# Kernel tuning notes

Hardware: AMD Instinct MI355X
Metric: run time of the kernel (lower is better)

Reference implementation:

```python
import jax, jax.numpy as jnp
import numpy as np

T = 2048
D_IN = 1024
D_OUT = 1024
N_HEAD = 16
HEAD_DIM = D_OUT // N_HEAD


def setup_inputs() -> dict:
    key = jax.random.key(0)
    kx, kq, kk, kv = jax.random.split(key, 4)
    s = 1.0 / np.sqrt(D_IN)
    return {
        "x": jax.random.normal(kx, (T, D_IN), dtype=jnp.float32),
        "W_q": jax.random.normal(kq, (D_OUT, D_IN), dtype=jnp.float32) * s,
        "W_k": jax.random.normal(kk, (D_OUT, D_IN), dtype=jnp.float32) * s,
        "W_v": jax.random.normal(kv, (D_OUT, D_IN), dtype=jnp.float32) * s,
    }


def reference(x, W_q, W_k, W_v):
    t = x.shape[0]
    # linear projections (torch Linear: y = x @ W.T), split into heads: [H, T, Dh]
    q = (x @ W_q.T).reshape(t, N_HEAD, HEAD_DIM).transpose(1, 0, 2)
    k = (x @ W_k.T).reshape(t, N_HEAD, HEAD_DIM).transpose(1, 0, 2)
    v = (x @ W_v.T).reshape(t, N_HEAD, HEAD_DIM).transpose(1, 0, 2)
    # raw scores [H, T, T]
    omega = jnp.einsum("hqd,hkd->hqk", q, k)
    causal = jnp.triu(jnp.ones((t, t), dtype=bool), k=1)
    omega = jnp.where(causal[None, :, :], -jnp.inf, omega)
    # NOTE: faithful to source quirk — divides by head_dim**(-0.5),
    # i.e. multiplies scores by sqrt(head_dim)
    att_w = jax.nn.softmax(omega * (HEAD_DIM ** 0.5), axis=-1)
    context = jnp.einsum("hqk,hkd->hqd", att_w, v)  # [H, T, Dh]
    return context.transpose(1, 0, 2).reshape(t, D_OUT)
```

## Files before the change

kernel.cpp:

```cpp
#include <hip/hip_runtime.h>
#include <hip/hip_bf16.h>


typedef __bf16 bf16x8 __attribute__((ext_vector_type(8)));
typedef __bf16 bf16x4 __attribute__((ext_vector_type(4)));
typedef float  f32x4  __attribute__((ext_vector_type(4)));
typedef float  f32x16 __attribute__((ext_vector_type(16)));
typedef unsigned int u32;
typedef u32 u32x2 __attribute__((ext_vector_type(2)));
typedef u32 u32x4 __attribute__((ext_vector_type(4)));

#define MFMA(a, b, c) __builtin_amdgcn_mfma_f32_16x16x32_bf16((a), (b), (c), 0, 0, 0)
#define MFMA32(a, b, c) __builtin_amdgcn_mfma_f32_32x32x16_bf16((a), (b), (c), 0, 0, 0)

#if __has_builtin(__builtin_amdgcn_exp2f)
#define EXP2F(x) __builtin_amdgcn_exp2f(x)
#else
#define EXP2F(x) exp2f(x)
#endif

constexpr int T = 2048, DIN = 1024, DOUT = 1024, NH = 16, DH = 64;
constexpr float SC = 11.5415603f;
constexpr float DEFER = 0.6931472f;

constexpr size_t SZ_XMAT = (size_t)T * DIN * 2;
constexpr size_t SZ_WMAT = (size_t)DOUT * DIN * 2;
constexpr size_t OFF_XH = 0;
constexpr size_t OFF_XL = OFF_XH + SZ_XMAT;
constexpr size_t OFF_QH = OFF_XL + SZ_XMAT;
constexpr size_t OFF_QL = OFF_QH + SZ_XMAT;
constexpr size_t OFF_KH = OFF_QL + SZ_XMAT;
constexpr size_t OFF_KL = OFF_KH + SZ_XMAT;
constexpr size_t OFF_VT = OFF_KL + SZ_XMAT;
constexpr size_t OFF_W  = OFF_VT + SZ_XMAT;

__device__ __forceinline__ void gload_lds16(const void* g, void* l) {
  __builtin_amdgcn_global_load_lds(
      (const __attribute__((address_space(1))) void*)g,
      (__attribute__((address_space(3))) void*)l, 16, 0, 0);
}

__device__ __forceinline__ float xor32f(float x, int hi) {
#if __has_builtin(__builtin_amdgcn_permlane32_swap)
  const u32 xu = __builtin_bit_cast(u32, x);
  const u32x2 rp = __builtin_amdgcn_permlane32_swap(xu, xu, false, false);
  return __builtin_bit_cast(float, hi ? rp[0] : rp[1]);
#else
  return __shfl_xor(x, 32, 64);
#endif
}

__global__ void split_all(const float* __restrict__ x, const float* __restrict__ wq,
                          const float* __restrict__ wk, const float* __restrict__ wv,
                          char* __restrict__ ws) {
  const int i = blockIdx.x * 256 + threadIdx.x;
  const float* src;
  __bf16 *hi, *lo;
  int off;
  if (i < T * DIN / 4) {
    src = x; off = i;
    hi = (__bf16*)(ws + OFF_XH);
    lo = (__bf16*)(ws + OFF_XL);
  } else {
    const int j = i - T * DIN / 4;
    const int z = j >> 18;
    off = j & 262143;
    src = (z == 0) ? wq : ((z == 1) ? wk : wv);
    hi = (__bf16*)(ws + OFF_W + (size_t)z * 2 * SZ_WMAT);
    lo = hi + (size_t)DOUT * DIN;
  }
  const f32x4 v = ((const f32x4*)src)[off];
  bf16x4 h, l;
#pragma unroll
  for (int j = 0; j < 4; ++j) {
    const float xv = v[j];
    const __bf16 hh = (__bf16)xv;
    h[j] = hh;
    l[j] = (__bf16)(xv - (float)hh);
  }
  ((bf16x4*)hi)[off] = h;
  ((bf16x4*)lo)[off] = l;
}

template <bool SPLIT>
__device__ __forceinline__ void proj_loop(const __bf16* __restrict__ Ah,
                                          const __bf16* __restrict__ Al,
                                          const __bf16* __restrict__ Bh,
                                          const __bf16* __restrict__ Bl,
                                          __bf16* lds, int tm, int tn, int lane,
                                          int wv, f32x4 (&acc)[4][4]) {
  constexpr int BUF = SPLIT ? 16384 : 8192;
  constexpr int BOFF = SPLIT ? 8192 : 4096;
  const int wm = wv >> 1, wn = wv & 1;
  const int q4 = lane >> 4, r16 = lane & 15;

  auto STAGE = [&](int ks, int buf) {
    const int k0 = ks * 32;
    __bf16* base = lds + buf * BUF;
#pragma unroll
    for (int j = 0; j < 2; ++j) {
      const int cbase = wv * 128 + j * 64;
      const int cidx = cbase + lane;
      const int row = cidx & 127, kc = cidx >> 7;
      const size_t ga = (size_t)(tm + row) * DIN + k0 + kc * 8;
      const size_t gb = (size_t)(tn + row) * DIN + k0 + kc * 8;
      gload_lds16(Ah + ga, base + cbase * 8);
      gload_lds16(Bh + gb, base + BOFF + cbase * 8);
      if constexpr (SPLIT) {
        gload_lds16(Al + ga, base + 4096 + cbase * 8);
        gload_lds16(Bl + gb, base + 12288 + cbase * 8);
      }
    }
  };

  STAGE(0, 0);
  STAGE(1, 1);

  for (int ks = 0; ks < 32; ++ks) {
    const int buf = ks & 1;
    if (ks < 31) {
      if constexpr (SPLIT) asm volatile("s_waitcnt vmcnt(8)" ::: "memory");
      else                 asm volatile("s_waitcnt vmcnt(4)" ::: "memory");
    } else {
      asm volatile("s_waitcnt vmcnt(0)" ::: "memory");
    }
    __builtin_amdgcn_s_barrier();
    __builtin_amdgcn_sched_barrier(0);

    const __bf16* ldsA = lds + buf * BUF;
    const __bf16* ldsB = ldsA + BOFF;

    bf16x8 fah[4], fbh[4], fal[4], fbl[4];
#pragma unroll
    for (int b = 0; b < 4; ++b) {
      const int ra = wm * 64 + b * 16 + r16;
      const int rb = wn * 64 + b * 16 + r16;
      fah[b] = *(const bf16x8*)(ldsA + (q4 * 128 + ra) * 8);
      fbh[b] = *(const bf16x8*)(ldsB + (q4 * 128 + rb) * 8);
      if constexpr (SPLIT) {
        fal[b] = *(const bf16x8*)(ldsA + 4096 + (q4 * 128 + ra) * 8);
        fbl[b] = *(const bf16x8*)(ldsB + 4096 + (q4 * 128 + rb) * 8);
      }
    }
    __builtin_amdgcn_s_setprio(1);
#pragma unroll
    for (int bm = 0; bm < 4; ++bm)
#pragma unroll
      for (int bn = 0; bn < 4; ++bn) {
        acc[bm][bn] = MFMA(fah[bm], fbh[bn], acc[bm][bn]);
        if constexpr (SPLIT) {
          acc[bm][bn] = MFMA(fah[bm], fbl[bn], acc[bm][bn]);
          acc[bm][bn] = MFMA(fal[bm], fbh[bn], acc[bm][bn]);
        }
      }
    __builtin_amdgcn_s_setprio(0);
    asm volatile("s_waitcnt lgkmcnt(0)" ::: "memory");
    __builtin_amdgcn_sched_barrier(0);
    __builtin_amdgcn_s_barrier();
    __builtin_amdgcn_sched_barrier(0);
    if (ks < 30) STAGE(ks + 2, buf);
  }
}

__global__ __launch_bounds__(256, 2) void qkv_proj(char* ws) {
  const int nb = (blockIdx.x & 7) * 48 + (blockIdx.x >> 3);
  const int z = nb >> 7;
  const int t_ = nb & 127;
  const int tm = (t_ >> 3) * 128;
  const int tn = (t_ & 7) * 128;
  const int tid = threadIdx.x;
  const int lane = tid & 63, wv = tid >> 6;
  const int wm = wv >> 1, wn = wv & 1;
  const int q4 = lane >> 4, r16 = lane & 15;

  const __bf16* Ah = (const __bf16*)(ws + OFF_XH);
  const __bf16* Al = (const __bf16*)(ws + OFF_XL);
  const __bf16* Bh = (const __bf16*)(ws + OFF_W + (size_t)z * 2 * SZ_WMAT);
  const __bf16* Bl = Bh + (size_t)DOUT * DIN;

  __shared__ alignas(16) __bf16 lds[32768];

  f32x4 acc[4][4] = {};

  if (z < 2) {
    proj_loop<true>(Ah, Al, Bh, Bl, lds, tm, tn, lane, wv, acc);
    __bf16* Oh = (__bf16*)(ws + (z == 0 ? OFF_QH : OFF_KH));
    __bf16* Ol = (__bf16*)(ws + (z == 0 ? OFF_QL : OFF_KL));
#pragma unroll
    for (int bm = 0; bm < 4; ++bm)
#pragma unroll
      for (int bn = 0; bn < 4; ++bn)
#pragma unroll
        for (int r = 0; r < 4; ++r) {
          const int t = tm + wm * 64 + bm * 16 + q4 * 4 + r;
          const int n = tn + wn * 64 + bn * 16 + r16;
          const float v = acc[bm][bn][r];
          const __bf16 hh = (__bf16)v;
          Oh[(size_t)t * DOUT + n] = hh;
          Ol[(size_t)t * DOUT + n] = (__bf16)(v - (float)hh);
        }
  } else {
    proj_loop<false>(Ah, Al, Bh, Bl, lds, tm, tn, lane, wv, acc);
    __syncthreads();
    __bf16* tb = lds;
#pragma unroll
    for (int bm = 0; bm < 4; ++bm)
#pragma unroll
      for (int bn = 0; bn < 4; ++bn)
#pragma unroll
        for (int r = 0; r < 4; ++r) {
          const int tl = wm * 64 + bm * 16 + q4 * 4 + r;
          const int nl = wn * 64 + bn * 16 + r16;
          tb[(size_t)nl * 136 + tl] = (__bf16)acc[bm][bn][r];
        }
    __syncthreads();
    __bf16* Vt = (__bf16*)(ws + OFF_VT);
#pragma unroll
    for (int it = 0; it < 8; ++it) {
      const int cid = it * 256 + tid;
      const int nl = cid >> 4, tc = cid & 15;
      const bf16x8 vd = *(const bf16x8*)(tb + (size_t)nl * 136 + tc * 8);
      *(bf16x8*)(Vt + (size_t)(tn + nl) * T + tm + tc * 8) = vd;
    }
  }
}

__global__ __launch_bounds__(256, 2) void attn_kernel(const char* __restrict__ ws,
                                                      float* __restrict__ out) {
  const int bid = blockIdx.x;
  const int h = bid & 15;
  const int qt = (bid < 256) ? (31 - (bid >> 4)) : ((bid - 256) >> 4);
  const int tid = threadIdx.x;
  const int lane = tid & 63, wid = tid >> 6;
  const int qhalf = wid & 1, kvpar = wid >> 1;
  const int r32 = lane & 31, hi = lane >> 5, hi8 = hi * 8;
  const int qg = qt * 64 + qhalf * 32 + r32;
  const int NT = qt + 1;
  const int mid = (NT + 1) >> 1;
  const int tBeg = kvpar ? mid : 0;
  const int tEnd = kvpar ? NT : mid;

  const __bf16* Qh = (const __bf16*)(ws + OFF_QH);
  const __bf16* Ql = (const __bf16*)(ws + OFF_QL);
  const __bf16* Kh = (const __bf16*)(ws + OFF_KH);
  const __bf16* Kl = (const __bf16*)(ws + OFF_KL);
  const __bf16* Vt = (const __bf16*)(ws + OFF_VT);

  __shared__ alignas(16) __bf16 sK[2][2][2][64 * 72];

  bf16x8 fqh[4], fql[4];
#pragma unroll
  for (int ds = 0; ds < 4; ++ds) {
    const size_t off = (size_t)qg * DOUT + h * 64 + ds * 16 + hi8;
    fqh[ds] = *(const bf16x8*)(Qh + off);
    fql[ds] = *(const bf16x8*)(Ql + off);
  }

  bf16x8 st[8];
  const int hid = qhalf * 64 + lane;
  auto ISSUE = [&](int t) {
    const int kv0 = t * 64;
#pragma unroll
    for (int j = 0; j < 4; ++j) {
      const int c = j * 128 + hid;
      const int row = c >> 3, dc = c & 7;
      const size_t ko = (size_t)(kv0 + row) * DOUT + h * 64 + dc * 8;
      st[j] = *(const bf16x8*)(Kh + ko);
      st[4 + j] = *(const bf16x8*)(Kl + ko);
    }
  };
  auto WRITE = [&](int b) {
#pragma unroll
    for (int j = 0; j < 4; ++j) {
      const int c = j * 128 + hid;
      const int row = c >> 3, dc = c & 7;
      *(bf16x8*)(&sK[kvpar][b][0][row * 72 + dc * 8]) = st[j];
      *(bf16x8*)(&sK[kvpar][b][1][row * 72 + dc * 8]) = st[4 + j];
    }
  };

  f32x16 acc0 = {}, acc1 = {};
  float mrun = -1e30f, lrun = 0.f;

  if (tBeg < tEnd) {
    ISSUE(tBeg);
    WRITE(0);
    if (tBeg + 1 < tEnd) ISSUE(tBeg + 1);
  }
  asm volatile("s_waitcnt lgkmcnt(0)" ::: "memory");
  __builtin_amdgcn_sched_barrier(0);
  __builtin_amdgcn_s_barrier();
  __builtin_amdgcn_sched_barrier(0);

  for (int it = 0; it < mid; ++it) {
    const int t = tBeg + it;
    const int p = it & 1;
    if (t < tEnd) {
      if (t + 1 < tEnd) {
        WRITE(p ^ 1);
        if (t + 2 < tEnd) ISSUE(t + 2);
      }

      const int kv0 = t * 64;
      const bool dodiag = (t == NT - 1);
      const bool do1 = !(dodiag && qhalf == 0);

      bf16x8 va0[4], va1[4];
#pragma unroll
      for (int ks = 0; ks < 4; ++ks) {
        const size_t vo = (size_t)(h * 64 + r32) * T + kv0 + ks * 16 + hi8;
        va0[ks] = *(const bf16x8*)(Vt + vo);
        va1[ks] = *(const bf16x8*)(Vt + vo + (size_t)32 * T);
      }

      const __bf16* kbh = &sK[kvpar][p][0][0];
      const __bf16* kbl = &sK[kvpar][p][1][0];
      f32x16 s0 = {}, s1 = {};
      __builtin_amdgcn_s_setprio(1);
#pragma unroll
      for (int ds = 0; ds < 4; ++ds) {
        const int ko = ds * 16 + hi8;
        const bf16x8 kh0 = *(const bf16x8*)(kbh + r32 * 72 + ko);
        const bf16x8 kl0 = *(const bf16x8*)(kbl + r32 * 72 + ko);
        s0 = MFMA32(kh0, fqh[ds], s0);
        s0 = MFMA32(kl0, fqh[ds], s0);
        s0 = MFMA32(kh0, fql[ds], s0);
      }
      if (do1) {
#pragma unroll
        for (int ds = 0; ds < 4; ++ds) {
          const int ko = ds * 16 + hi8;
          const bf16x8 kh1 = *(const bf16x8*)(kbh + (32 + r32) * 72 + ko);
          const bf16x8 kl1 = *(const bf16x8*)(kbl + (32 + r32) * 72 + ko);
          s1 = MFMA32(kh1, fqh[ds], s1);
          s1 = MFMA32(kl1, fqh[ds], s1);
          s1 = MFMA32(kh1, fql[ds], s1);
        }
      }
      __builtin_amdgcn_s_setprio(0);

      if (dodiag) {
#pragma unroll
        for (int r = 0; r < 16; ++r) {
          const int kr = (r & 3) + 8 * (r >> 2) + 4 * hi;
          if (kv0 + kr > qg) s0[r] = -1e30f;
          if (kv0 + 32 + kr > qg) s1[r] = -1e30f;
        }
      }

      float mx = -1e30f;
#pragma unroll
      for (int r = 0; r < 16; ++r) {
        mx = fmaxf(mx, s0[r]);
        mx = fmaxf(mx, s1[r]);
      }
      mx = fmaxf(mx, xor32f(mx, hi));

      if (__any(mx - mrun > DEFER)) {
        const float mnew = fmaxf(mrun, mx);
        const float scale = EXP2F((mrun - mnew) * SC);
        mrun = mnew;
        lrun *= scale;
#pragma unroll
        for (int r = 0; r < 16; ++r) {
          acc0[r] *= scale;
          acc1[r] *= scale;
        }
      }
      const float mn2 = mrun * SC;

      float ps = 0.f;
#pragma unroll
      for (int r = 0; r < 16; ++r) {
        s0[r] = EXP2F(__builtin_fmaf(s0[r], SC, -mn2));
        s1[r] = EXP2F(__builtin_fmaf(s1[r], SC, -mn2));
        ps += s0[r] + s1[r];
      }
      ps += xor32f(ps, hi);
      lrun += ps;

      bf16x8 pb[4];
#pragma unroll
      for (int ks = 0; ks < 4; ++ks) {
        const int rb = (ks & 1) * 8;
        bf16x4 lo4, hi4;
#pragma unroll
        for (int j = 0; j < 4; ++j) {
          const float pl = (ks < 2) ? s0[rb + j] : s1[rb + j];
          const float ph = (ks < 2) ? s0[rb + 4 + j] : s1[rb + 4 + j];
          lo4[j] = (__bf16)pl;
          hi4[j] = (__bf16)ph;
        }
        const u32x2 L = __builtin_bit_cast(u32x2, lo4);
        const u32x2 H = __builtin_bit_cast(u32x2, hi4);
        u32x4 f;
#if __has_builtin(__builtin_amdgcn_permlane32_swap)
#pragma unroll
        for (int q = 0; q < 2; ++q) {
          const u32x2 rp = __builtin_amdgcn_permlane32_swap(L[q], H[q], false, false);
          f[q] = rp[0];
          f[2 + q] = rp[1];
        }
#else
#pragma unroll
        for (int q = 0; q < 2; ++q) {
          const u32 send = hi ? L[q] : H[q];
          const u32 recv = (u32)__shfl_xor((int)send, 32, 64);
          f[q] = hi ? recv : L[q];
          f[2 + q] = hi ? H[q] : recv;
        }
#endif
        pb[ks] = __builtin_bit_cast(bf16x8, f);
      }

      __builtin_amdgcn_s_setprio(1);
#pragma unroll
      for (int ks = 0; ks < 4; ++ks) {
        acc0 = MFMA32(va0[ks], pb[ks], acc0);
        acc1 = MFMA32(va1[ks], pb[ks], acc1);
      }
      __builtin_amdgcn_s_setprio(0);
    }

    asm volatile("s_waitcnt lgkmcnt(0)" ::: "memory");
    __builtin_amdgcn_sched_barrier(0);
    __builtin_amdgcn_s_barrier();
    __builtin_amdgcn_sched_barrier(0);
  }

  float* mg = (float*)&sK[0][0][0][0];
  if (kvpar == 1) {
    float* p = mg + (qhalf * 64 + lane) * 34;
    p[0] = mrun;
    p[1] = lrun;
#pragma unroll
    for (int r = 0; r < 16; ++r) {
      p[2 + r] = acc0[r];
      p[18 + r] = acc1[r];
    }
  }
  asm volatile("s_waitcnt lgkmcnt(0)" ::: "memory");
  __builtin_amdgcn_s_barrier();
  if (kvpar == 0) {
    const float* p = mg + (qhalf * 64 + lane) * 34;
    const float m1 = p[0], l1 = p[1];
    const float M = fmaxf(mrun, m1);
    const float w0 = EXP2F((mrun - M) * SC);
    const float w1 = EXP2F((m1 - M) * SC);
    const float rl = 1.0f / (lrun * w0 + l1 * w1);
#pragma unroll
    for (int r = 0; r < 16; ++r) {
      const int d = (r & 3) + 8 * (r >> 2) + 4 * hi;
      out[(size_t)qg * DOUT + h * 64 + d] = (acc0[r] * w0 + p[2 + r] * w1) * rl;
      out[(size_t)qg * DOUT + h * 64 + 32 + d] = (acc1[r] * w0 + p[18 + r] * w1) * rl;
    }
  }
}

extern "C" void kernel_launch(void* const* d_in, const int* in_sizes, int n_in,
                              void* d_out, int out_size, void* d_ws, size_t ws_size,
                              hipStream_t stream) {
  const float* x  = (const float*)d_in[0];
  const float* Wq = (const float*)d_in[1];
  const float* Wk = (const float*)d_in[2];
  const float* Wv = (const float*)d_in[3];
  char* ws = (char*)d_ws;

  split_all<<<5120, 256, 0, stream>>>(x, Wq, Wk, Wv, ws);
  qkv_proj<<<384, 256, 0, stream>>>(ws);
  attn_kernel<<<512, 256, 0, stream>>>(ws, (float*)d_out);
}
```

Measured before the change: 112.4 us.

## Split V projection into smaller 64x128 tiles and drop block swizzle

The V projection blocks now use 64x128 tiles with a dedicated single-precision bf16 loop, doubling the V block count so the grid grows from 384 to 512 blocks. Q/K blocks keep the split-precision 128x128 path in a specialized non-templated loop. The previous XCD-oriented block index swizzle is removed, and Q/K blocks now occupy the first 256 indices. The intent is to balance work, since the cheap V tiles previously finished early and left CUs idle, and to fill the GPU better. In exchange the V tiles get less data reuse per block and the L2 locality from the swizzle is lost.

```diff
diff --git a/kernel.cpp b/kernel.cpp
--- a/kernel.cpp
+++ b/kernel.cpp
@@ -82,15 +82,13 @@
   ((bf16x4*)lo)[off] = l;
 }
 
-template <bool SPLIT>
-__device__ __forceinline__ void proj_loop(const __bf16* __restrict__ Ah,
-                                          const __bf16* __restrict__ Al,
-                                          const __bf16* __restrict__ Bh,
-                                          const __bf16* __restrict__ Bl,
-                                          __bf16* lds, int tm, int tn, int lane,
-                                          int wv, f32x4 (&acc)[4][4]) {
-  constexpr int BUF = SPLIT ? 16384 : 8192;
-  constexpr int BOFF = SPLIT ? 8192 : 4096;
+__device__ __forceinline__ void proj_loop_qk(const __bf16* __restrict__ Ah,
+                                             const __bf16* __restrict__ Al,
+                                             const __bf16* __restrict__ Bh,
+                                             const __bf16* __restrict__ Bl,
+                                             __bf16* lds, int tm, int tn, int lane,
+                                             int wv, f32x4 (&acc)[4][4]) {
+  constexpr int BUF = 16384, BOFF = 8192;
   const int wm = wv >> 1, wn = wv & 1;
   const int q4 = lane >> 4, r16 = lane & 15;
 
@@ -106,10 +104,8 @@
       const size_t gb = (size_t)(tn + row) * DIN + k0 + kc * 8;
       gload_lds16(Ah + ga, base + cbase * 8);
       gload_lds16(Bh + gb, base + BOFF + cbase * 8);
-      if constexpr (SPLIT) {
-        gload_lds16(Al + ga, base + 4096 + cbase * 8);
-        gload_lds16(Bl + gb, base + 12288 + cbase * 8);
-      }
+      gload_lds16(Al + ga, base + 4096 + cbase * 8);
+      gload_lds16(Bl + gb, base + 12288 + cbase * 8);
     }
   };
 
@@ -118,12 +114,8 @@
 
   for (int ks = 0; ks < 32; ++ks) {
     const int buf = ks & 1;
-    if (ks < 31) {
-      if constexpr (SPLIT) asm volatile("s_waitcnt vmcnt(8)" ::: "memory");
-      else                 asm volatile("s_waitcnt vmcnt(4)" ::: "memory");
-    } else {
-      asm volatile("s_waitcnt vmcnt(0)" ::: "memory");
-    }
+    if (ks < 31) asm volatile("s_waitcnt vmcnt(8)" ::: "memory");
+    else         asm volatile("s_waitcnt vmcnt(0)" ::: "memory");
     __builtin_amdgcn_s_barrier();
     __builtin_amdgcn_sched_barrier(0);
 
@@ -137,10 +129,8 @@
       const int rb = wn * 64 + b * 16 + r16;
       fah[b] = *(const bf16x8*)(ldsA + (q4 * 128 + ra) * 8);
       fbh[b] = *(const bf16x8*)(ldsB + (q4 * 128 + rb) * 8);
-      if constexpr (SPLIT) {
-        fal[b] = *(const bf16x8*)(ldsA + 4096 + (q4 * 128 + ra) * 8);
-        fbl[b] = *(const bf16x8*)(ldsB + 4096 + (q4 * 128 + rb) * 8);
-      }
+      fal[b] = *(const bf16x8*)(ldsA + 4096 + (q4 * 128 + ra) * 8);
+      fbl[b] = *(const bf16x8*)(ldsB + 4096 + (q4 * 128 + rb) * 8);
     }
     __builtin_amdgcn_s_setprio(1);
 #pragma unroll
@@ -148,10 +138,8 @@
 #pragma unroll
       for (int bn = 0; bn < 4; ++bn) {
         acc[bm][bn] = MFMA(fah[bm], fbh[bn], acc[bm][bn]);
-        if constexpr (SPLIT) {
-          acc[bm][bn] = MFMA(fah[bm], fbl[bn], acc[bm][bn]);
-          acc[bm][bn] = MFMA(fal[bm], fbh[bn], acc[bm][bn]);
-        }
+        acc[bm][bn] = MFMA(fah[bm], fbl[bn], acc[bm][bn]);
+        acc[bm][bn] = MFMA(fal[bm], fbh[bn], acc[bm][bn]);
       }
     __builtin_amdgcn_s_setprio(0);
     asm volatile("s_waitcnt lgkmcnt(0)" ::: "memory");
@@ -163,27 +151,28 @@
 }
 
 __global__ __launch_bounds__(256, 2) void qkv_proj(char* ws) {
-  const int nb = (blockIdx.x & 7) * 48 + (blockIdx.x >> 3);
-  const int z = nb >> 7;
-  const int t_ = nb & 127;
-  const int tm = (t_ >> 3) * 128;
-  const int tn = (t_ & 7) * 128;
+  const int bid = blockIdx.x;
   const int tid = threadIdx.x;
   const int lane = tid & 63, wv = tid >> 6;
-  const int wm = wv >> 1, wn = wv & 1;
   const int q4 = lane >> 4, r16 = lane & 15;
+
+  __shared__ alignas(16) __bf16 lds[32768];
 
   const __bf16* Ah = (const __bf16*)(ws + OFF_XH);
   const __bf16* Al = (const __bf16*)(ws + OFF_XL);
-  const __bf16* Bh = (const __bf16*)(ws + OFF_W + (size_t)z * 2 * SZ_WMAT);
-  const __bf16* Bl = Bh + (size_t)DOUT * DIN;
-
-  __shared__ alignas(16) __bf16 lds[32768];
-
-  f32x4 acc[4][4] = {};
-
-  if (z < 2) {
-    proj_loop<true>(Ah, Al, Bh, Bl, lds, tm, tn, lane, wv, acc);
+
+  if (bid < 256) {
+    const int z = bid >> 7;
+    const int t_ = bid & 127;
+    const int tm = (t_ >> 3) * 128;
+    const int tn = (t_ & 7) * 128;
+    const int wm = wv >> 1, wn = wv & 1;
+    const __bf16* Bh = (const __bf16*)(ws + OFF_W + (size_t)z * 2 * SZ_WMAT);
+    const __bf16* Bl = Bh + (size_t)DOUT * DIN;
+
+    f32x4 acc[4][4] = {};
+    proj_loop_qk(Ah, Al, Bh, Bl, lds, tm, tn, lane, wv, acc);
+
     __bf16* Oh = (__bf16*)(ws + (z == 0 ? OFF_QH : OFF_KH));
     __bf16* Ol = (__bf16*)(ws + (z == 0 ? OFF_QL : OFF_KL));
 #pragma unroll
@@ -200,26 +189,82 @@
           Ol[(size_t)t * DOUT + n] = (__bf16)(v - (float)hh);
         }
   } else {
-    proj_loop<false>(Ah, Al, Bh, Bl, lds, tm, tn, lane, wv, acc);
+    const int vt = bid - 256;
+    const int tm = (vt >> 3) * 64;
+    const int tn = (vt & 7) * 128;
+    const __bf16* Bh = (const __bf16*)(ws + OFF_W + 2 * 2 * SZ_WMAT);
+
+    auto STAGE = [&](int ks, int buf) {
+      const int k0 = ks * 32;
+      __bf16* base = lds + buf * 6144;
+      {
+        const int cbase = wv * 64;
+        const int c = cbase + lane;
+        const int row = c & 63, kc = c >> 6;
+        gload_lds16(Ah + (size_t)(tm + row) * DIN + k0 + kc * 8, base + cbase * 8);
+      }
+#pragma unroll
+      for (int j = 0; j < 2; ++j) {
+        const int cbase = wv * 128 + j * 64;
+        const int c = cbase + lane;
+        const int row = c & 127, kc = c >> 7;
+        gload_lds16(Bh + (size_t)(tn + row) * DIN + k0 + kc * 8,
+                    base + 2048 + cbase * 8);
+      }
+    };
+
+    f32x4 acc[4][2] = {};
+    STAGE(0, 0);
+    STAGE(1, 1);
+    for (int ks = 0; ks < 32; ++ks) {
+      const int buf = ks & 1;
+      if (ks < 31) asm volatile("s_waitcnt vmcnt(3)" ::: "memory");
+      else         asm volatile("s_waitcnt vmcnt(0)" ::: "memory");
+      __builtin_amdgcn_s_barrier();
+      __builtin_amdgcn_sched_barrier(0);
+
+      const __bf16* ldsA = lds + buf * 6144;
+      const __bf16* ldsB = ldsA + 2048;
+      bf16x8 fa[4], fb[2];
+#pragma unroll
+      for (int b = 0; b < 4; ++b)
+        fa[b] = *(const bf16x8*)(ldsA + (q4 * 64 + b * 16 + r16) * 8);
+#pragma unroll
+      for (int b = 0; b < 2; ++b)
+        fb[b] = *(const bf16x8*)(ldsB + (q4 * 128 + wv * 32 + b * 16 + r16) * 8);
+      __builtin_amdgcn_s_setprio(1);
+#pragma unroll
+      for (int bm = 0; bm < 4; ++bm)
+#pragma unroll
+        for (int bn = 0; bn < 2; ++bn)
+          acc[bm][bn] = MFMA(fa[bm], fb[bn], acc[bm][bn]);
+      __builtin_amdgcn_s_setprio(0);
+      asm volatile("s_waitcnt lgkmcnt(0)" ::: "memory");
+      __builtin_amdgcn_sched_barrier(0);
+      __builtin_amdgcn_s_barrier();
+      __builtin_amdgcn_sched_barrier(0);
+      if (ks < 30) STAGE(ks + 2, buf);
+    }
+
     __syncthreads();
     __bf16* tb = lds;
 #pragma unroll
     for (int bm = 0; bm < 4; ++bm)
 #pragma unroll
-      for (int bn = 0; bn < 4; ++bn)
+      for (int bn = 0; bn < 2; ++bn)
 #pragma unroll
         for (int r = 0; r < 4; ++r) {
-          const int tl = wm * 64 + bm * 16 + q4 * 4 + r;
-          const int nl = wn * 64 + bn * 16 + r16;
-          tb[(size_t)nl * 136 + tl] = (__bf16)acc[bm][bn][r];
+          const int tl = bm * 16 + q4 * 4 + r;
+          const int nl = wv * 32 + bn * 16 + r16;
+          tb[(size_t)nl * 72 + tl] = (__bf16)acc[bm][bn][r];
         }
     __syncthreads();
     __bf16* Vt = (__bf16*)(ws + OFF_VT);
 #pragma unroll
-    for (int it = 0; it < 8; ++it) {
+    for (int it = 0; it < 4; ++it) {
       const int cid = it * 256 + tid;
-      const int nl = cid >> 4, tc = cid & 15;
-      const bf16x8 vd = *(const bf16x8*)(tb + (size_t)nl * 136 + tc * 8);
+      const int nl = cid >> 3, tc = cid & 7;
+      const bf16x8 vd = *(const bf16x8*)(tb + (size_t)nl * 72 + tc * 8);
       *(bf16x8*)(Vt + (size_t)(tn + nl) * T + tm + tc * 8) = vd;
     }
   }
@@ -467,6 +512,6 @@
   char* ws = (char*)d_ws;
 
   split_all<<<5120, 256, 0, stream>>>(x, Wq, Wk, Wv, ws);
-  qkv_proj<<<384, 256, 0, stream>>>(ws);
+  qkv_proj<<<512, 256, 0, stream>>>(ws);
   attn_kernel<<<512, 256, 0, stream>>>(ws, (float*)d_out);
 }
```

Measured after the change: 95.21 us (median of 2 runs). 1.18x faster.
